# Kernel tuning notes

Measured on AMD Instinct MI355X. Metric: run time of the kernel, lower is better.

The kernel has to match this reference:

```python
import jax, jax.numpy as jnp
import numpy as np

N = 65536   # nodes
E = 262144  # edges
IN = 16     # input node feat dim
H0 = 16     # layer0 out dim
H1 = 8      # layer1 out dim (H0 // 2)
EA = 10     # edge attr dim (hardcoded in edge_nn)


def setup_inputs() -> dict:
    key = jax.random.key(0)
    ks = jax.random.split(key, 12)
    s = 0.05
    return {
        "x": jax.random.normal(ks[0], (N, IN), jnp.float32),
        "edge_index": jax.random.randint(ks[1], (2, E), 0, N),
        "edge_attr": jax.random.normal(ks[2], (E, EA), jnp.float32),
        # layer 0 edge MLP: Linear(10, 256) -> ReLU -> Linear(256, IN*H0)
        "w1_0": jax.random.normal(ks[3], (EA, H0 * H0), jnp.float32) * s,
        "b1_0": jnp.zeros((H0 * H0,), jnp.float32),
        "w2_0": jax.random.normal(ks[4], (H0 * H0, IN * H0), jnp.float32) * s,
        "b2_0": jnp.zeros((IN * H0,), jnp.float32),
        "root_0": jax.random.normal(ks[5], (IN, H0), jnp.float32) * s,
        "bias_0": jnp.zeros((H0,), jnp.float32),
        # layer 1 edge MLP: Linear(10, 256) -> ReLU -> Linear(256, H0*H1)
        "w1_1": jax.random.normal(ks[6], (EA, H0 * H0), jnp.float32) * s,
        "b1_1": jnp.zeros((H0 * H0,), jnp.float32),
        "w2_1": jax.random.normal(ks[7], (H0 * H0, H0 * H1), jnp.float32) * s,
        "b2_1": jnp.zeros((H0 * H1,), jnp.float32),
        "root_1": jax.random.normal(ks[8], (H0, H1), jnp.float32) * s,
        "bias_1": jnp.zeros((H1,), jnp.float32),
        # final edge classifier fc: Linear(2*H1, 1)
        "fc_w": jax.random.normal(ks[9], (2 * H1, 1), jnp.float32) * s,
        "fc_b": jnp.zeros((1,), jnp.float32),
    }


def _nnconv(x, src, dst, edge_attr, w1, b1, w2, b2, root, bias, in_c, out_c):
    # edge-conditioned weight generation: MLP(edge_attr) -> [E, in_c, out_c]
    h = jax.nn.relu(edge_attr @ w1 + b1)                 # [E, hid]
    We = (h @ w2 + b2).reshape(-1, in_c, out_c)          # [E, in, out]
    msg = jnp.einsum('ei,eio->eo', x[src], We)           # per-edge matmul [E, out]
    ssum = jax.ops.segment_sum(msg, dst, num_segments=N)               # [N, out]
    cnt = jax.ops.segment_sum(jnp.ones((msg.shape[0],), msg.dtype), dst, num_segments=N)
    agg = ssum / jnp.maximum(cnt, 1.0)[:, None]          # scatter-mean
    return agg + x @ root + bias                         # root transform + bias


def reference(x, edge_index, edge_attr, w1_0, b1_0, w2_0, b2_0, root_0, bias_0,
              w1_1, b1_1, w2_1, b2_1, root_1, bias_1, fc_w, fc_b):
    src, dst = edge_index[0], edge_index[1]
    # dropout is identity in eval mode
    x = jax.nn.relu(_nnconv(x, src, dst, edge_attr, w1_0, b1_0, w2_0, b2_0, root_0, bias_0, IN, H0))
    x = jax.nn.relu(_nnconv(x, src, dst, edge_attr, w1_1, b1_1, w2_1, b2_1, root_1, bias_1, H0, H1))
    ef = jnp.concatenate([x[src], x[dst]], axis=-1)      # [E, 2*H1]
    return jax.nn.sigmoid(ef @ fc_w + fc_b)              # [E, 1]
```

## Files before the change

kernel.cpp:

```cpp
#include <hip/hip_runtime.h>
#include <stdint.h>

#define NN 65536
#define NE 262144

typedef __attribute__((ext_vector_type(8))) short bf16x8;
typedef __attribute__((ext_vector_type(4))) float f32x4;

__device__ __forceinline__ short f2bf(float f) {
  union { float f; uint32_t u; } v; v.f = f;
  uint32_t u = v.u + 0x7fffu + ((v.u >> 16) & 1u);
  return (short)(u >> 16);
}
__device__ __forceinline__ uint32_t cvtpk(float lo, float hi) {
  uint32_t r;
  asm("v_cvt_pk_bf16_f32 %0, %1, %2" : "=v"(r) : "v"(lo), "v"(hi));
  return r;
}

__global__ __launch_bounds__(256) void prep_all(
    const float* __restrict__ ea, short* __restrict__ eab,
    const float* __restrict__ w1_0, const float* __restrict__ w1_1,
    const float* __restrict__ w2_0, const float* __restrict__ w2_1,
    short* __restrict__ w1t0, short* __restrict__ w1t1,
    short* __restrict__ w2t0, short* __restrict__ w2t1) {
  int idx = blockIdx.x * 256 + threadIdx.x;
  {
    int e = idx >> 4, k = idx & 15;
    eab[idx] = (k < 10) ? f2bf(ea[e * 10 + k]) : (short)0;
  }
  if (idx < 65536) {
    if (idx < 8192) {
      int n = idx >> 5, k = idx & 31;
      w1t0[idx] = (k < 10) ? f2bf(w1_0[k * 256 + n]) : (short)0;
      w1t1[idx] = (k < 10) ? f2bf(w1_1[k * 256 + n]) : (short)0;
    }
    if (idx < 32768) {
      int n = idx >> 8, k = idx & 255;
      w2t1[idx] = f2bf(w2_1[k * 128 + n]);
    }
    {
      int n = idx >> 8, k = idx & 255;
      w2t0[idx] = f2bf(w2_0[k * 256 + n]);
    }
  }
}

__global__ __launch_bounds__(256) void hist_kernel(const int* __restrict__ ei,
                                                   int* __restrict__ cnt32) {
  int e = blockIdx.x * 256 + threadIdx.x;
  atomicAdd(&cnt32[ei[NE + e]], 1);
}

__global__ __launch_bounds__(256) void scan1_kernel(const int* __restrict__ cnt32,
                                                    int* __restrict__ bsum) {
  __shared__ int sd[256];
  int t = threadIdx.x, b = blockIdx.x;
  sd[t] = cnt32[b * 256 + t];
  __syncthreads();
  for (int s = 128; s > 0; s >>= 1) {
    if (t < s) sd[t] += sd[t + s];
    __syncthreads();
  }
  if (t == 0) bsum[b] = sd[0];
}

__global__ __launch_bounds__(256) void scan2_kernel(const int* __restrict__ bsum,
                                                    int* __restrict__ boff) {
  __shared__ int sd[256];
  int t = threadIdx.x;
  int v = bsum[t];
  sd[t] = v;
  __syncthreads();
  for (int st = 1; st < 256; st <<= 1) {
    int x = (t >= st) ? sd[t - st] : 0;
    __syncthreads();
    sd[t] += x;
    __syncthreads();
  }
  boff[t] = sd[t] - v;
}

__global__ __launch_bounds__(256) void scan3_kernel(const int* __restrict__ cnt32,
                                                    const int* __restrict__ boff,
                                                    int* __restrict__ off) {
  __shared__ int sd[256];
  int t = threadIdx.x, b = blockIdx.x;
  int idx = b * 256 + t;
  int v = cnt32[idx];
  sd[t] = v;
  __syncthreads();
  for (int st = 1; st < 256; st <<= 1) {
    int x = (t >= st) ? sd[t - st] : 0;
    __syncthreads();
    sd[t] += x;
    __syncthreads();
  }
  off[idx] = boff[b] + sd[t] - v;
  if (b == 255 && t == 255) off[65536] = boff[255] + sd[255];
}

__global__ __launch_bounds__(256) void scatter_kernel(const int* __restrict__ ei,
                                                      int* __restrict__ cursor,
                                                      int* __restrict__ eidx) {
  int e = blockIdx.x * 256 + threadIdx.x;
  int pos = atomicAdd(&cursor[ei[NE + e]], 1);
  eidx[pos] = e;
}

template <int N2, int OUTC>
__global__ __launch_bounds__(512, 4) void edge_kernel(
    const float* __restrict__ x, const int* __restrict__ ei,
    const short* __restrict__ eab, const short* __restrict__ w1t,
    const float* __restrict__ b1, const short* __restrict__ w2t,
    const float* __restrict__ b2, float* __restrict__ msg) {
  constexpr int WCOLS = N2 / 8;
  constexpr int NT2 = WCOLS / 16;
  constexpr int LOGO = (OUTC == 16) ? 4 : 3;
  constexpr int PADO = OUTC + 1;
  constexpr int PARTSZ = 8 * 128 * PADO * 4;
  constexpr int XSOFF = (PARTSZ > 65536) ? PARTSZ : 65536;
  __shared__ alignas(16) char smem[XSOFF + 128 * 20 * 4];
  char* const hB = smem;
  float* const partial = (float*)smem;
  float* const xs = (float*)(smem + XSOFF);

  const int tid = threadIdx.x;
  const int w = tid >> 6;
  const int lane = tid & 63;
  const int g = lane >> 4;
  const int lr = lane & 15;
  const int e0 = blockIdx.x * 128;

  const int eR = tid >> 2;
  const int qR = tid & 3;
  {
    int s = ei[e0 + eR];
    float4 v = *(const float4*)(x + (size_t)s * 16 + qR * 4);
    *(float4*)(xs + eR * 20 + qR * 4) = v;
  }

  bf16x8 aw[2];
#pragma unroll
  for (int ml = 0; ml < 2; ++ml)
    aw[ml] = *(const bf16x8*)(w1t + ((w * 2 + ml) * 16 + lr) * 32 + g * 8);
  bf16x8 be[8];
#pragma unroll
  for (int et = 0; et < 8; ++et) {
    if (g < 2)
      be[et] = *(const bf16x8*)(eab + (size_t)(e0 + et * 16 + lr) * 16 + g * 8);
    else
      be[et] = (bf16x8){0, 0, 0, 0, 0, 0, 0, 0};
  }

  f32x4 acc1[2][8];
#pragma unroll
  for (int ml = 0; ml < 2; ++ml)
#pragma unroll
    for (int et = 0; et < 8; ++et) acc1[ml][et] = (f32x4){0.f, 0.f, 0.f, 0.f};
#pragma unroll
  for (int et = 0; et < 8; ++et)
#pragma unroll
    for (int ml = 0; ml < 2; ++ml)
      acc1[ml][et] = __builtin_amdgcn_mfma_f32_16x16x32_bf16(aw[ml], be[et], acc1[ml][et], 0, 0, 0);

  bf16x8 bcur[NT2];
#pragma unroll
  for (int nt = 0; nt < NT2; ++nt) {
    int colo = w * WCOLS + nt * 16 + lr;
    bcur[nt] = *(const bf16x8*)(w2t + colo * 256 + g * 8);
  }

#pragma unroll
  for (int ml = 0; ml < 2; ++ml) {
    int kb = (w * 2 + ml) * 16 + g * 4;
    float4 bb = *(const float4*)(b1 + kb);
#pragma unroll
    for (int et = 0; et < 8; ++et) {
      int e = et * 16 + lr;
      float v0 = fmaxf(acc1[ml][et][0] + bb.x, 0.f);
      float v1 = fmaxf(acc1[ml][et][1] + bb.y, 0.f);
      float v2 = fmaxf(acc1[ml][et][2] + bb.z, 0.f);
      float v3 = fmaxf(acc1[ml][et][3] + bb.w, 0.f);
      int2 pw; pw.x = (int)cvtpk(v0, v1); pw.y = (int)cvtpk(v2, v3);
      *(int2*)(hB + ((e * 512 + kb * 2) ^ ((e & 7) << 4))) = pw;
    }
  }
  __syncthreads();

  f32x4 acc[8][NT2];
#pragma unroll
  for (int mt = 0; mt < 8; ++mt)
#pragma unroll
    for (int nt = 0; nt < NT2; ++nt) acc[mt][nt] = (f32x4){0.f, 0.f, 0.f, 0.f};
#pragma unroll
  for (int ks = 0; ks < 8; ++ks) {
    bf16x8 bnxt[NT2];
    if (ks < 7) {
#pragma unroll
      for (int nt = 0; nt < NT2; ++nt) {
        int colo = w * WCOLS + nt * 16 + lr;
        bnxt[nt] = *(const bf16x8*)(w2t + colo * 256 + (ks + 1) * 32 + g * 8);
      }
    }
#pragma unroll
    for (int hf = 0; hf < 2; ++hf) {
      bf16x8 a2[4];
#pragma unroll
      for (int m4 = 0; m4 < 4; ++m4) {
        int e = (hf * 4 + m4) * 16 + lr;
        a2[m4] = *(const bf16x8*)(hB + ((e * 512 + ks * 64 + g * 16) ^ ((e & 7) << 4)));
      }
#pragma unroll
      for (int nt = 0; nt < NT2; ++nt)
#pragma unroll
        for (int m4 = 0; m4 < 4; ++m4)
          acc[hf * 4 + m4][nt] =
              __builtin_amdgcn_mfma_f32_16x16x32_bf16(a2[m4], bcur[nt], acc[hf * 4 + m4][nt], 0, 0, 0);
    }
    if (ks < 7) {
#pragma unroll
      for (int nt = 0; nt < NT2; ++nt) bcur[nt] = bnxt[nt];
    }
  }
  __syncthreads();

  {
    const int o = lr & (OUTC - 1);
    float b2c[NT2];
    int iv[NT2];
#pragma unroll
    for (int nt = 0; nt < NT2; ++nt) {
      int colo = w * WCOLS + nt * 16 + lr;
      b2c[nt] = b2[colo];
      iv[nt] = colo >> LOGO;
    }
#pragma unroll
    for (int mt = 0; mt < 8; ++mt)
#pragma unroll
      for (int r = 0; r < 4; ++r) {
        int e = mt * 16 + g * 4 + r;
        float m = 0.f;
#pragma unroll
        for (int nt = 0; nt < NT2; ++nt)
          m += (acc[mt][nt][r] + b2c[nt]) * xs[e * 20 + iv[nt]];
        if (OUTC == 8) m += __shfl_xor(m, 8, 64);
        partial[((size_t)w * 128 + e) * PADO + o] = m;
      }
  }
  __syncthreads();

  if (qR * 4 < OUTC) {
    float v[4];
#pragma unroll
    for (int j = 0; j < 4; ++j) {
      int o = qR * 4 + j;
      float s = 0.f;
#pragma unroll
      for (int sl = 0; sl < 8; ++sl) s += partial[((size_t)sl * 128 + eR) * PADO + o];
      v[j] = s;
    }
    *(float4*)(msg + (size_t)(e0 + eR) * OUTC + qR * 4) =
        (float4){v[0], v[1], v[2], v[3]};
  }
}

template <int OUTC>
__global__ __launch_bounds__(256) void node_csr(
    const float* __restrict__ xin, const float* __restrict__ msg,
    const int* __restrict__ off, const int* __restrict__ eidx,
    const float* __restrict__ root, const float* __restrict__ bias,
    float* __restrict__ xout) {
  constexpr int Q = OUTC / 4;
  __shared__ float rootL[16 * OUTC];
  __shared__ float biasL[OUTC];
  int tid = threadIdx.x;
  if (tid < 16 * OUTC) rootL[tid] = root[tid];
  if (tid < OUTC) biasL[tid] = bias[tid];
  __syncthreads();
  int n = blockIdx.x * (256 / Q) + tid / Q;
  int q = tid & (Q - 1);
  int o0 = off[n], o1 = off[n + 1];
  const float4* msg4 = (const float4*)msg;
  float s[4] = {0.f, 0.f, 0.f, 0.f};
  for (int i = o0; i < o1; ++i) {
    int e = eidx[i];
    float4 v = msg4[(size_t)e * Q + q];
    s[0] += v.x; s[1] += v.y; s[2] += v.z; s[3] += v.w;
  }
  float inv = 1.0f / fmaxf((float)(o1 - o0), 1.0f);
  float xi[16];
#pragma unroll
  for (int i = 0; i < 4; ++i) {
    float4 v = ((const float4*)(xin + (size_t)n * 16))[i];
    xi[4 * i] = v.x; xi[4 * i + 1] = v.y; xi[4 * i + 2] = v.z; xi[4 * i + 3] = v.w;
  }
  float r[4];
#pragma unroll
  for (int j = 0; j < 4; ++j) {
    int o = q * 4 + j;
    float a = s[j] * inv + biasL[o];
#pragma unroll
    for (int i = 0; i < 16; ++i) a += xi[i] * rootL[i * OUTC + o];
    r[j] = fmaxf(a, 0.f);
  }
  *(float4*)(xout + (size_t)n * OUTC + q * 4) = (float4){r[0], r[1], r[2], r[3]};
}

__global__ __launch_bounds__(256) void final_kernel(
    const float* __restrict__ x2, const int* __restrict__ ei,
    const float* __restrict__ fcw, const float* __restrict__ fcb,
    float* __restrict__ out) {
  int e = blockIdx.x * 256 + threadIdx.x;
  int s = ei[e], d = ei[NE + e];
  float acc = fcb[0];
  const float* xsr = x2 + (size_t)s * 8;
  const float* xdr = x2 + (size_t)d * 8;
#pragma unroll
  for (int c = 0; c < 8; ++c) acc += xsr[c] * fcw[c];
#pragma unroll
  for (int c = 0; c < 8; ++c) acc += xdr[c] * fcw[8 + c];
  out[e] = 1.0f / (1.0f + __expf(-acc));
}

extern "C" void kernel_launch(void* const* d_in, const int* in_sizes, int n_in,
                              void* d_out, int out_size, void* d_ws, size_t ws_size,
                              hipStream_t stream) {
  const float* x      = (const float*)d_in[0];
  const int*   ei     = (const int*)d_in[1];
  const float* ea     = (const float*)d_in[2];
  const float* w1_0   = (const float*)d_in[3];
  const float* b1_0   = (const float*)d_in[4];
  const float* w2_0   = (const float*)d_in[5];
  const float* b2_0   = (const float*)d_in[6];
  const float* root_0 = (const float*)d_in[7];
  const float* bias_0 = (const float*)d_in[8];
  const float* w1_1   = (const float*)d_in[9];
  const float* b1_1   = (const float*)d_in[10];
  const float* w2_1   = (const float*)d_in[11];
  const float* b2_1   = (const float*)d_in[12];
  const float* root_1 = (const float*)d_in[13];
  const float* bias_1 = (const float*)d_in[14];
  const float* fc_w   = (const float*)d_in[15];
  const float* fc_b   = (const float*)d_in[16];
  float* out = (float*)d_out;

  char* ws = (char*)d_ws;
  int*   off    = (int*)(ws);
  int*   cursor = (int*)(ws + (512u << 10));
  int*   bsum   = (int*)(ws + (1u << 20));
  int*   boff   = (int*)(ws + (1u << 20) + 4096);
  short* w1t0   = (short*)(ws + (1u << 20) + 16384);
  short* w1t1   = w1t0 + 8192;
  short* w2t0   = w1t1 + 8192;
  short* w2t1   = w2t0 + 65536;
  float* x1     = (float*)(ws + (2u << 20));
  float* x2     = (float*)(ws + (6u << 20));
  int*   eidx   = (int*)(ws + (8u << 20));
  short* eab    = (short*)(ws + (9u << 20));
  float* msg    = (float*)(ws + (17u << 20));

  int* cnt32 = cursor;

  hipMemsetAsync(cnt32, 0, (size_t)NN * 4, stream);
  prep_all<<<NE * 16 / 256, 256, 0, stream>>>(ea, eab, w1_0, w1_1, w2_0, w2_1,
                                              w1t0, w1t1, w2t0, w2t1);
  hist_kernel<<<NE / 256, 256, 0, stream>>>(ei, cnt32);
  scan1_kernel<<<256, 256, 0, stream>>>(cnt32, bsum);
  scan2_kernel<<<1, 256, 0, stream>>>(bsum, boff);
  scan3_kernel<<<256, 256, 0, stream>>>(cnt32, boff, off);
  hipMemcpyAsync(cursor, off, (size_t)NN * 4, hipMemcpyDeviceToDevice, stream);
  scatter_kernel<<<NE / 256, 256, 0, stream>>>(ei, cursor, eidx);

  edge_kernel<256, 16><<<NE / 128, 512, 0, stream>>>(
      x, ei, eab, w1t0, b1_0, w2t0, b2_0, msg);
  node_csr<16><<<NN * 4 / 256, 256, 0, stream>>>(x, msg, off, eidx, root_0, bias_0, x1);
  edge_kernel<128, 8><<<NE / 128, 512, 0, stream>>>(
      x1, ei, eab, w1t1, b1_1, w2t1, b2_1, msg);
  node_csr<8><<<NN * 2 / 256, 256, 0, stream>>>(x1, msg, off, eidx, root_1, bias_1, x2);
  final_kernel<<<NE / 256, 256, 0, stream>>>(x2, ei, fc_w, fc_b, out);
}
```

Before: 179.8 us.

## Retile edge GEMM into 2x4 warp grid and fold histogram and cursor copy

```diff
diff --git a/kernel.cpp b/kernel.cpp
--- a/kernel.cpp
+++ b/kernel.cpp
@@ -23,12 +23,14 @@
     const float* __restrict__ w1_0, const float* __restrict__ w1_1,
     const float* __restrict__ w2_0, const float* __restrict__ w2_1,
     short* __restrict__ w1t0, short* __restrict__ w1t1,
-    short* __restrict__ w2t0, short* __restrict__ w2t1) {
+    short* __restrict__ w2t0, short* __restrict__ w2t1,
+    const int* __restrict__ ei, int* __restrict__ cnt32) {
   int idx = blockIdx.x * 256 + threadIdx.x;
   {
     int e = idx >> 4, k = idx & 15;
     eab[idx] = (k < 10) ? f2bf(ea[e * 10 + k]) : (short)0;
   }
+  if (idx < NE) atomicAdd(&cnt32[ei[NE + idx]], 1);
   if (idx < 65536) {
     if (idx < 8192) {
       int n = idx >> 5, k = idx & 31;
@@ -44,12 +46,6 @@
       w2t0[idx] = f2bf(w2_0[k * 256 + n]);
     }
   }
-}
-
-__global__ __launch_bounds__(256) void hist_kernel(const int* __restrict__ ei,
-                                                   int* __restrict__ cnt32) {
-  int e = blockIdx.x * 256 + threadIdx.x;
-  atomicAdd(&cnt32[ei[NE + e]], 1);
 }
 
 __global__ __launch_bounds__(256) void scan1_kernel(const int* __restrict__ cnt32,
@@ -83,7 +79,8 @@
 
 __global__ __launch_bounds__(256) void scan3_kernel(const int* __restrict__ cnt32,
                                                     const int* __restrict__ boff,
-                                                    int* __restrict__ off) {
+                                                    int* __restrict__ off,
+                                                    int* __restrict__ cursor) {
   __shared__ int sd[256];
   int t = threadIdx.x, b = blockIdx.x;
   int idx = b * 256 + t;
@@ -96,7 +93,9 @@
     sd[t] += x;
     __syncthreads();
   }
-  off[idx] = boff[b] + sd[t] - v;
+  int o = boff[b] + sd[t] - v;
+  off[idx] = o;
+  cursor[idx] = o;
   if (b == 255 && t == 255) off[65536] = boff[255] + sd[255];
 }
 
@@ -114,16 +113,14 @@
     const short* __restrict__ eab, const short* __restrict__ w1t,
     const float* __restrict__ b1, const short* __restrict__ w2t,
     const float* __restrict__ b2, float* __restrict__ msg) {
-  constexpr int WCOLS = N2 / 8;
-  constexpr int NT2 = WCOLS / 16;
+  constexpr int WC = N2 / 4;
+  constexpr int NT2 = WC / 16;
   constexpr int LOGO = (OUTC == 16) ? 4 : 3;
   constexpr int PADO = OUTC + 1;
-  constexpr int PARTSZ = 8 * 128 * PADO * 4;
-  constexpr int XSOFF = (PARTSZ > 65536) ? PARTSZ : 65536;
-  __shared__ alignas(16) char smem[XSOFF + 128 * 20 * 4];
-  char* const hB = smem;
+  __shared__ alignas(16) char smem[65536 + 128 * 20 * 4];
+  short* const hB = (short*)smem;
   float* const partial = (float*)smem;
-  float* const xs = (float*)(smem + XSOFF);
+  float* const xs = (float*)(smem + 65536);
 
   const int tid = threadIdx.x;
   const int w = tid >> 6;
@@ -131,6 +128,8 @@
   const int g = lane >> 4;
   const int lr = lane & 15;
   const int e0 = blockIdx.x * 128;
+  const int er = w >> 2;
+  const int cg = w & 3;
 
   const int eR = tid >> 2;
   const int qR = tid & 3;
@@ -167,14 +166,17 @@
   bf16x8 bcur[NT2];
 #pragma unroll
   for (int nt = 0; nt < NT2; ++nt) {
-    int colo = w * WCOLS + nt * 16 + lr;
+    int colo = cg * WC + nt * 16 + lr;
     bcur[nt] = *(const bf16x8*)(w2t + colo * 256 + g * 8);
   }
 
 #pragma unroll
   for (int ml = 0; ml < 2; ++ml) {
-    int kb = (w * 2 + ml) * 16 + g * 4;
-    float4 bb = *(const float4*)(b1 + kb);
+    const int K16 = w * 2 + ml;
+    const int ks2 = K16 >> 1;
+    const int g2 = (K16 & 1) * 2 + (g >> 1);
+    const int j0 = (g & 1) * 4;
+    float4 bb = *(const float4*)(b1 + K16 * 16 + g * 4);
 #pragma unroll
     for (int et = 0; et < 8; ++et) {
       int e = et * 16 + lr;
@@ -183,14 +185,14 @@
       float v2 = fmaxf(acc1[ml][et][2] + bb.z, 0.f);
       float v3 = fmaxf(acc1[ml][et][3] + bb.w, 0.f);
       int2 pw; pw.x = (int)cvtpk(v0, v1); pw.y = (int)cvtpk(v2, v3);
-      *(int2*)(hB + ((e * 512 + kb * 2) ^ ((e & 7) << 4))) = pw;
-    }
-  }
-  __syncthreads();
-
-  f32x4 acc[8][NT2];
-#pragma unroll
-  for (int mt = 0; mt < 8; ++mt)
+      *(int2*)(hB + ((ks2 * 4 + g2) * 128 + e) * 8 + j0) = pw;
+    }
+  }
+  __syncthreads();
+
+  f32x4 acc[4][NT2];
+#pragma unroll
+  for (int mt = 0; mt < 4; ++mt)
 #pragma unroll
     for (int nt = 0; nt < NT2; ++nt) acc[mt][nt] = (f32x4){0.f, 0.f, 0.f, 0.f};
 #pragma unroll
@@ -199,25 +201,21 @@
     if (ks < 7) {
 #pragma unroll
       for (int nt = 0; nt < NT2; ++nt) {
-        int colo = w * WCOLS + nt * 16 + lr;
+        int colo = cg * WC + nt * 16 + lr;
         bnxt[nt] = *(const bf16x8*)(w2t + colo * 256 + (ks + 1) * 32 + g * 8);
       }
     }
-#pragma unroll
-    for (int hf = 0; hf < 2; ++hf) {
-      bf16x8 a2[4];
-#pragma unroll
-      for (int m4 = 0; m4 < 4; ++m4) {
-        int e = (hf * 4 + m4) * 16 + lr;
-        a2[m4] = *(const bf16x8*)(hB + ((e * 512 + ks * 64 + g * 16) ^ ((e & 7) << 4)));
-      }
-#pragma unroll
-      for (int nt = 0; nt < NT2; ++nt)
-#pragma unroll
-        for (int m4 = 0; m4 < 4; ++m4)
-          acc[hf * 4 + m4][nt] =
-              __builtin_amdgcn_mfma_f32_16x16x32_bf16(a2[m4], bcur[nt], acc[hf * 4 + m4][nt], 0, 0, 0);
-    }
+    bf16x8 a2[4];
+#pragma unroll
+    for (int mt = 0; mt < 4; ++mt) {
+      int e = er * 64 + mt * 16 + lr;
+      a2[mt] = *(const bf16x8*)(hB + ((ks * 4 + g) * 128 + e) * 8);
+    }
+#pragma unroll
+    for (int nt = 0; nt < NT2; ++nt)
+#pragma unroll
+      for (int mt = 0; mt < 4; ++mt)
+        acc[mt][nt] = __builtin_amdgcn_mfma_f32_16x16x32_bf16(a2[mt], bcur[nt], acc[mt][nt], 0, 0, 0);
     if (ks < 7) {
 #pragma unroll
       for (int nt = 0; nt < NT2; ++nt) bcur[nt] = bnxt[nt];
@@ -231,21 +229,21 @@
     int iv[NT2];
 #pragma unroll
     for (int nt = 0; nt < NT2; ++nt) {
-      int colo = w * WCOLS + nt * 16 + lr;
+      int colo = cg * WC + nt * 16 + lr;
       b2c[nt] = b2[colo];
       iv[nt] = colo >> LOGO;
     }
 #pragma unroll
-    for (int mt = 0; mt < 8; ++mt)
+    for (int mt = 0; mt < 4; ++mt)
 #pragma unroll
       for (int r = 0; r < 4; ++r) {
-        int e = mt * 16 + g * 4 + r;
+        int e = er * 64 + mt * 16 + g * 4 + r;
         float m = 0.f;
 #pragma unroll
         for (int nt = 0; nt < NT2; ++nt)
           m += (acc[mt][nt][r] + b2c[nt]) * xs[e * 20 + iv[nt]];
         if (OUTC == 8) m += __shfl_xor(m, 8, 64);
-        partial[((size_t)w * 128 + e) * PADO + o] = m;
+        partial[((size_t)cg * 128 + e) * PADO + o] = m;
       }
   }
   __syncthreads();
@@ -257,7 +255,7 @@
       int o = qR * 4 + j;
       float s = 0.f;
 #pragma unroll
-      for (int sl = 0; sl < 8; ++sl) s += partial[((size_t)sl * 128 + eR) * PADO + o];
+      for (int sl = 0; sl < 4; ++sl) s += partial[((size_t)sl * 128 + eR) * PADO + o];
       v[j] = s;
     }
     *(float4*)(msg + (size_t)(e0 + eR) * OUTC + qR * 4) =
@@ -364,12 +362,10 @@
 
   hipMemsetAsync(cnt32, 0, (size_t)NN * 4, stream);
   prep_all<<<NE * 16 / 256, 256, 0, stream>>>(ea, eab, w1_0, w1_1, w2_0, w2_1,
-                                              w1t0, w1t1, w2t0, w2t1);
-  hist_kernel<<<NE / 256, 256, 0, stream>>>(ei, cnt32);
+                                              w1t0, w1t1, w2t0, w2t1, ei, cnt32);
   scan1_kernel<<<256, 256, 0, stream>>>(cnt32, bsum);
   scan2_kernel<<<1, 256, 0, stream>>>(bsum, boff);
-  scan3_kernel<<<256, 256, 0, stream>>>(cnt32, boff, off);
-  hipMemcpyAsync(cursor, off, (size_t)NN * 4, hipMemcpyDeviceToDevice, stream);
+  scan3_kernel<<<256, 256, 0, stream>>>(cnt32, boff, off, cursor);
   scatter_kernel<<<NE / 256, 256, 0, stream>>>(ei, cursor, eidx);
 
   edge_kernel<256, 16><<<NE / 128, 512, 0, stream>>>(
```

Measured after the change: 222.7 us. 23.9% more time.

## Fuse histogram into prep, drop cursor memcpy, use fragment-native LDS layout

Applied to the files above, without the earlier changes.

```diff
diff --git a/kernel.cpp b/kernel.cpp
--- a/kernel.cpp
+++ b/kernel.cpp
@@ -23,12 +23,14 @@
     const float* __restrict__ w1_0, const float* __restrict__ w1_1,
     const float* __restrict__ w2_0, const float* __restrict__ w2_1,
     short* __restrict__ w1t0, short* __restrict__ w1t1,
-    short* __restrict__ w2t0, short* __restrict__ w2t1) {
+    short* __restrict__ w2t0, short* __restrict__ w2t1,
+    const int* __restrict__ ei, int* __restrict__ cnt32) {
   int idx = blockIdx.x * 256 + threadIdx.x;
   {
     int e = idx >> 4, k = idx & 15;
     eab[idx] = (k < 10) ? f2bf(ea[e * 10 + k]) : (short)0;
   }
+  if (idx < NE) atomicAdd(&cnt32[ei[NE + idx]], 1);
   if (idx < 65536) {
     if (idx < 8192) {
       int n = idx >> 5, k = idx & 31;
@@ -44,12 +46,6 @@
       w2t0[idx] = f2bf(w2_0[k * 256 + n]);
     }
   }
-}
-
-__global__ __launch_bounds__(256) void hist_kernel(const int* __restrict__ ei,
-                                                   int* __restrict__ cnt32) {
-  int e = blockIdx.x * 256 + threadIdx.x;
-  atomicAdd(&cnt32[ei[NE + e]], 1);
 }
 
 __global__ __launch_bounds__(256) void scan1_kernel(const int* __restrict__ cnt32,
@@ -83,7 +79,8 @@
 
 __global__ __launch_bounds__(256) void scan3_kernel(const int* __restrict__ cnt32,
                                                     const int* __restrict__ boff,
-                                                    int* __restrict__ off) {
+                                                    int* __restrict__ off,
+                                                    int* __restrict__ cursor) {
   __shared__ int sd[256];
   int t = threadIdx.x, b = blockIdx.x;
   int idx = b * 256 + t;
@@ -96,7 +93,9 @@
     sd[t] += x;
     __syncthreads();
   }
-  off[idx] = boff[b] + sd[t] - v;
+  int o = boff[b] + sd[t] - v;
+  off[idx] = o;
+  cursor[idx] = o;
   if (b == 255 && t == 255) off[65536] = boff[255] + sd[255];
 }
 
@@ -121,7 +120,7 @@
   constexpr int PARTSZ = 8 * 128 * PADO * 4;
   constexpr int XSOFF = (PARTSZ > 65536) ? PARTSZ : 65536;
   __shared__ alignas(16) char smem[XSOFF + 128 * 20 * 4];
-  char* const hB = smem;
+  short* const hB = (short*)smem;
   float* const partial = (float*)smem;
   float* const xs = (float*)(smem + XSOFF);
 
@@ -173,17 +172,18 @@
 
 #pragma unroll
   for (int ml = 0; ml < 2; ++ml) {
-    int kb = (w * 2 + ml) * 16 + g * 4;
-    float4 bb = *(const float4*)(b1 + kb);
+    const int K16 = w * 2 + ml;
+    const int rg = ml * 2 + (g >> 1);
+    const int j0 = (g & 1) * 4;
+    float4 bb1 = *(const float4*)(b1 + K16 * 16 + g * 4);
 #pragma unroll
     for (int et = 0; et < 8; ++et) {
-      int e = et * 16 + lr;
-      float v0 = fmaxf(acc1[ml][et][0] + bb.x, 0.f);
-      float v1 = fmaxf(acc1[ml][et][1] + bb.y, 0.f);
-      float v2 = fmaxf(acc1[ml][et][2] + bb.z, 0.f);
-      float v3 = fmaxf(acc1[ml][et][3] + bb.w, 0.f);
+      float v0 = fmaxf(acc1[ml][et][0] + bb1.x, 0.f);
+      float v1 = fmaxf(acc1[ml][et][1] + bb1.y, 0.f);
+      float v2 = fmaxf(acc1[ml][et][2] + bb1.z, 0.f);
+      float v3 = fmaxf(acc1[ml][et][3] + bb1.w, 0.f);
       int2 pw; pw.x = (int)cvtpk(v0, v1); pw.y = (int)cvtpk(v2, v3);
-      *(int2*)(hB + ((e * 512 + kb * 2) ^ ((e & 7) << 4))) = pw;
+      *(int2*)(hB + ((et * 8 + w) * 64 + rg * 16 + lr) * 8 + j0) = pw;
     }
   }
   __syncthreads();
@@ -207,10 +207,8 @@
     for (int hf = 0; hf < 2; ++hf) {
       bf16x8 a2[4];
 #pragma unroll
-      for (int m4 = 0; m4 < 4; ++m4) {
-        int e = (hf * 4 + m4) * 16 + lr;
-        a2[m4] = *(const bf16x8*)(hB + ((e * 512 + ks * 64 + g * 16) ^ ((e & 7) << 4)));
-      }
+      for (int m4 = 0; m4 < 4; ++m4)
+        a2[m4] = *(const bf16x8*)(hB + (((hf * 4 + m4) * 8 + ks) * 64 + lane) * 8);
 #pragma unroll
       for (int nt = 0; nt < NT2; ++nt)
 #pragma unroll
@@ -364,12 +362,10 @@
 
   hipMemsetAsync(cnt32, 0, (size_t)NN * 4, stream);
   prep_all<<<NE * 16 / 256, 256, 0, stream>>>(ea, eab, w1_0, w1_1, w2_0, w2_1,
-                                              w1t0, w1t1, w2t0, w2t1);
-  hist_kernel<<<NE / 256, 256, 0, stream>>>(ei, cnt32);
+                                              w1t0, w1t1, w2t0, w2t1, ei, cnt32);
   scan1_kernel<<<256, 256, 0, stream>>>(cnt32, bsum);
   scan2_kernel<<<1, 256, 0, stream>>>(bsum, boff);
-  scan3_kernel<<<256, 256, 0, stream>>>(cnt32, boff, off);
-  hipMemcpyAsync(cursor, off, (size_t)NN * 4, hipMemcpyDeviceToDevice, stream);
+  scan3_kernel<<<256, 256, 0, stream>>>(cnt32, boff, off, cursor);
   scatter_kernel<<<NE / 256, 256, 0, stream>>>(ei, cursor, eidx);
 
   edge_kernel<256, 16><<<NE / 128, 512, 0, stream>>>(
```

Result: faster. 165.3 us (-8.1%).
